# Optimization experiments

Hardware: AMD Instinct MI355X
Metric: run time of the kernel (lower is better)

The kernel has to match this reference:

```python
import jax, jax.numpy as jnp
import numpy as np

DELTA = 0.1      # delta from __init__
LN_EPS = 1e-5    # torch LayerNorm default eps

B, IN, OUT, E = 256, 512, 512, 256


def setup_inputs() -> dict:
    key = jax.random.key(0)
    ks = jax.random.split(key, 6)
    return {
        "x": jax.random.normal(ks[0], (B, IN), dtype=jnp.float32),
        # nn.init.normal_(std=0.1), shape (out_features, in_features)
        "weights": 0.1 * jax.random.normal(ks[1], (OUT, IN), dtype=jnp.float32),
        # frozen predicate embeddings (in_features, embedding_dim)
        "pred_emb": jax.random.normal(ks[2], (IN, E), dtype=jnp.float32),
        # nn.Linear(E, OUT): weight (OUT, E), bias (OUT,)
        "attn_w": jax.random.uniform(ks[3], (OUT, E), dtype=jnp.float32,
                                      minval=-1.0, maxval=1.0) / np.sqrt(E),
        "attn_b": jax.random.uniform(ks[4], (OUT,), dtype=jnp.float32,
                                      minval=-1.0, maxval=1.0) / np.sqrt(E),
        # nn.LayerNorm(OUT)
        "ln_g": jnp.ones((OUT,), dtype=jnp.float32),
        "ln_b": jnp.zeros((OUT,), dtype=jnp.float32),
    }


def _layernorm(s, g, b):
    mu = s.mean(axis=-1, keepdims=True)
    var = ((s - mu) ** 2).mean(axis=-1, keepdims=True)
    return (s - mu) * jax.lax.rsqrt(var + LN_EPS) * g + b


def reference(x, weights, pred_emb, attn_w, attn_b, ln_g, ln_b):
    # semantic attention gate: batch-invariant, compute once -> (IN, OUT)
    scores = pred_emb @ attn_w.T + attn_b                    # (IN, OUT)
    sig = jax.nn.sigmoid(_layernorm(scores, ln_g, ln_b))     # (IN, OUT)

    xe = x[:, :, None]                                       # (B, IN, 1)
    wt = weights.T[None]                                     # (1, IN, OUT)
    # abs_weight * attn_adjusted, fused elementwise -> (B, IN, OUT)
    aw = jnp.abs(xe * wt) * (sig[None] * xe)

    bias = aw.max(axis=1) - aw.sum(axis=1)                   # CONJUNCTION: max - sum
    return x @ weights.T + DELTA * bias                      # (B, OUT)
```

## Files before the change

kernel.cpp:

```cpp
#include <hip/hip_runtime.h>
#include <math.h>

#define B_   256
#define IN_  512
#define OUT_ 512
#define E_   256
#define DELTA_ 0.1f
#define LN_EPS_ 1e-5f

__global__ __launch_bounds__(512)
void k1_scores_ln_sig(const float* __restrict__ pred_emb,
                      const float* __restrict__ attn_w,
                      const float* __restrict__ attn_b,
                      const float* __restrict__ ln_g,
                      const float* __restrict__ ln_b,
                      const float* __restrict__ weights,
                      float* __restrict__ wA,
                      float* __restrict__ vA) {
    __shared__ float pe[4][E_];
    __shared__ float red[8][4][2];
    __shared__ float smu[4], srs[4];

    const int t    = threadIdx.x;
    const int lane = t & 63;
    const int wid  = t >> 6;
    const int i0   = blockIdx.x * 4;
    const int o    = t;

    #pragma unroll
    for (int k = 0; k < 2; ++k) {
        int p = t + 512 * k;
        pe[p >> 8][p & 255] = pred_emb[(size_t)(i0 + (p >> 8)) * E_ + (p & 255)];
    }
    __syncthreads();

    const float4* p0 = reinterpret_cast<const float4*>(pe[0]);
    const float4* p1 = reinterpret_cast<const float4*>(pe[1]);
    const float4* p2 = reinterpret_cast<const float4*>(pe[2]);
    const float4* p3 = reinterpret_cast<const float4*>(pe[3]);
    const float4* wrow = reinterpret_cast<const float4*>(attn_w + (size_t)o * E_);

    float a0 = 0.f, a1 = 0.f, a2 = 0.f, a3 = 0.f;
    #pragma unroll 8
    for (int e4 = 0; e4 < E_ / 4; ++e4) {
        float4 w4 = wrow[e4];
        float4 q0 = p0[e4];
        float4 q1 = p1[e4];
        float4 q2 = p2[e4];
        float4 q3 = p3[e4];
        a0 += q0.x * w4.x + q0.y * w4.y + q0.z * w4.z + q0.w * w4.w;
        a1 += q1.x * w4.x + q1.y * w4.y + q1.z * w4.z + q1.w * w4.w;
        a2 += q2.x * w4.x + q2.y * w4.y + q2.z * w4.z + q2.w * w4.w;
        a3 += q3.x * w4.x + q3.y * w4.y + q3.z * w4.z + q3.w * w4.w;
    }
    const float bo = attn_b[o];
    a0 += bo; a1 += bo; a2 += bo; a3 += bo;

    {
        float s10 = a0, s20 = a0 * a0;
        float s11 = a1, s21 = a1 * a1;
        float s12 = a2, s22 = a2 * a2;
        float s13 = a3, s23 = a3 * a3;
        #pragma unroll
        for (int off = 32; off > 0; off >>= 1) {
            s10 += __shfl_down(s10, off); s20 += __shfl_down(s20, off);
            s11 += __shfl_down(s11, off); s21 += __shfl_down(s21, off);
            s12 += __shfl_down(s12, off); s22 += __shfl_down(s22, off);
            s13 += __shfl_down(s13, off); s23 += __shfl_down(s23, off);
        }
        if (lane == 0) {
            red[wid][0][0] = s10; red[wid][0][1] = s20;
            red[wid][1][0] = s11; red[wid][1][1] = s21;
            red[wid][2][0] = s12; red[wid][2][1] = s22;
            red[wid][3][0] = s13; red[wid][3][1] = s23;
        }
    }
    __syncthreads();
    if (t < 4) {
        float s1 = 0.f, s2 = 0.f;
        #pragma unroll
        for (int w = 0; w < 8; ++w) { s1 += red[w][t][0]; s2 += red[w][t][1]; }
        float mu  = s1 / (float)OUT_;
        float var = s2 / (float)OUT_ - mu * mu;
        smu[t] = mu;
        srs[t] = rsqrtf(var + LN_EPS_);
    }
    __syncthreads();

    const float g  = ln_g[o];
    const float bb = ln_b[o];
    float z0 = (a0 - smu[0]) * srs[0] * g + bb;
    float z1 = (a1 - smu[1]) * srs[1] * g + bb;
    float z2 = (a2 - smu[2]) * srs[2] * g + bb;
    float z3 = (a3 - smu[3]) * srs[3] * g + bb;
    float sg0 = 1.f / (1.f + expf(-z0));
    float sg1 = 1.f / (1.f + expf(-z1));
    float sg2 = 1.f / (1.f + expf(-z2));
    float sg3 = 1.f / (1.f + expf(-z3));

    float4 w4 = *reinterpret_cast<const float4*>(weights + (size_t)o * IN_ + i0);
    wA[(size_t)(i0 + 0) * OUT_ + o] = w4.x;
    wA[(size_t)(i0 + 1) * OUT_ + o] = w4.y;
    wA[(size_t)(i0 + 2) * OUT_ + o] = w4.z;
    wA[(size_t)(i0 + 3) * OUT_ + o] = w4.w;
    vA[(size_t)(i0 + 0) * OUT_ + o] = DELTA_ * fabsf(w4.x) * sg0;
    vA[(size_t)(i0 + 1) * OUT_ + o] = DELTA_ * fabsf(w4.y) * sg1;
    vA[(size_t)(i0 + 2) * OUT_ + o] = DELTA_ * fabsf(w4.z) * sg2;
    vA[(size_t)(i0 + 3) * OUT_ + o] = DELTA_ * fabsf(w4.w) * sg3;
}

#define K2_SK 8
#define K2_CH 64
#define K2_BO (B_ * OUT_)

__global__ __launch_bounds__(256)
void k2_partials(const float* __restrict__ x,
                 const float* __restrict__ wA,
                 const float* __restrict__ vA,
                 float* __restrict__ plin,
                 float* __restrict__ pmax) {
    __shared__ float4 xs [64 * 17];
    __shared__ float4 wss[64 * 17];
    __shared__ float4 vss[64 * 17];

    const int t  = threadIdx.x;
    const int oq = t & 15;
    const int br = t >> 4;
    const int o0 = blockIdx.x * 64;
    const int b0 = blockIdx.y * 64;
    const int i0 = blockIdx.z * K2_CH;

    #pragma unroll
    for (int k = 0; k < 4; ++k) {
        int p   = t + k * 256;
        int row = p >> 4;
        int c4  = p & 15;
        xs [row * 17 + c4] = *reinterpret_cast<const float4*>(
            x  + (size_t)(b0 + row) * IN_  + i0 + c4 * 4);
        wss[row * 17 + c4] = *reinterpret_cast<const float4*>(
            wA + (size_t)(i0 + row) * OUT_ + o0 + c4 * 4);
        vss[row * 17 + c4] = *reinterpret_cast<const float4*>(
            vA + (size_t)(i0 + row) * OUT_ + o0 + c4 * 4);
    }
    __syncthreads();

    float d[4][4], s[4][4], m[4][4];
    #pragma unroll
    for (int b = 0; b < 4; ++b)
        #pragma unroll
        for (int oo = 0; oo < 4; ++oo) {
            d[b][oo] = 0.f; s[b][oo] = 0.f; m[b][oo] = -INFINITY;
        }

    #pragma unroll 2
    for (int i4 = 0; i4 < K2_CH / 4; ++i4) {
        float4 xv0 = xs[(br +  0) * 17 + i4];
        float4 xv1 = xs[(br + 16) * 17 + i4];
        float4 xv2 = xs[(br + 32) * 17 + i4];
        float4 xv3 = xs[(br + 48) * 17 + i4];
        float xr[4][4] = {{xv0.x, xv0.y, xv0.z, xv0.w},
                          {xv1.x, xv1.y, xv1.z, xv1.w},
                          {xv2.x, xv2.y, xv2.z, xv2.w},
                          {xv3.x, xv3.y, xv3.z, xv3.w}};
        float ur[4][4];
        #pragma unroll
        for (int b = 0; b < 4; ++b)
            #pragma unroll
            for (int ii = 0; ii < 4; ++ii)
                ur[b][ii] = xr[b][ii] * fabsf(xr[b][ii]);

        #pragma unroll
        for (int ii = 0; ii < 4; ++ii) {
            float4 w4 = wss[(i4 * 4 + ii) * 17 + oq];
            float4 v4 = vss[(i4 * 4 + ii) * 17 + oq];
            #pragma unroll
            for (int b = 0; b < 4; ++b) {
                float xb = xr[b][ii];
                float ub = ur[b][ii];
                float p_;
                d[b][0] = fmaf(xb, w4.x, d[b][0]); p_ = ub * v4.x; s[b][0] += p_; m[b][0] = fmaxf(m[b][0], p_);
                d[b][1] = fmaf(xb, w4.y, d[b][1]); p_ = ub * v4.y; s[b][1] += p_; m[b][1] = fmaxf(m[b][1], p_);
                d[b][2] = fmaf(xb, w4.z, d[b][2]); p_ = ub * v4.z; s[b][2] += p_; m[b][2] = fmaxf(m[b][2], p_);
                d[b][3] = fmaf(xb, w4.w, d[b][3]); p_ = ub * v4.w; s[b][3] += p_; m[b][3] = fmaxf(m[b][3], p_);
            }
        }
    }

    #pragma unroll
    for (int b = 0; b < 4; ++b) {
        const int row = b0 + br + 16 * b;
        const size_t idx = ((size_t)blockIdx.z * B_ + row) * OUT_ + o0 + oq * 4;
        *reinterpret_cast<float4*>(plin + idx) =
            make_float4(d[b][0] - s[b][0], d[b][1] - s[b][1],
                        d[b][2] - s[b][2], d[b][3] - s[b][3]);
        *reinterpret_cast<float4*>(pmax + idx) =
            make_float4(m[b][0], m[b][1], m[b][2], m[b][3]);
    }
}

__global__ __launch_bounds__(256)
void k3_combine(const float4* __restrict__ plin4,
                const float4* __restrict__ pmax4,
                float4* __restrict__ out4) {
    const int g = blockIdx.x * 256 + threadIdx.x;
    const int Q = K2_BO / 4;
    float4 l  = plin4[g];
    float4 mx = pmax4[g];
    #pragma unroll
    for (int p = 1; p < K2_SK; ++p) {
        float4 lp = plin4[(size_t)p * Q + g];
        float4 mp = pmax4[(size_t)p * Q + g];
        l.x += lp.x; l.y += lp.y; l.z += lp.z; l.w += lp.w;
        mx.x = fmaxf(mx.x, mp.x); mx.y = fmaxf(mx.y, mp.y);
        mx.z = fmaxf(mx.z, mp.z); mx.w = fmaxf(mx.w, mp.w);
    }
    out4[g] = make_float4(l.x + mx.x, l.y + mx.y, l.z + mx.z, l.w + mx.w);
}

extern "C" void kernel_launch(void* const* d_in, const int* in_sizes, int n_in,
                              void* d_out, int out_size, void* d_ws, size_t ws_size,
                              hipStream_t stream) {
    const float* x        = (const float*)d_in[0];
    const float* weights  = (const float*)d_in[1];
    const float* pred_emb = (const float*)d_in[2];
    const float* attn_w   = (const float*)d_in[3];
    const float* attn_b   = (const float*)d_in[4];
    const float* ln_g     = (const float*)d_in[5];
    const float* ln_b     = (const float*)d_in[6];

    float* wA   = (float*)d_ws;
    float* vA   = wA + (size_t)IN_ * OUT_;
    float* plin = vA + (size_t)IN_ * OUT_;
    float* pmax = plin + (size_t)K2_SK * K2_BO;

    k1_scores_ln_sig<<<IN_ / 4, 512, 0, stream>>>(
        pred_emb, attn_w, attn_b, ln_g, ln_b, weights, wA, vA);

    k2_partials<<<dim3(OUT_ / 64, B_ / 64, K2_SK), 256, 0, stream>>>(
        x, wA, vA, plin, pmax);

    k3_combine<<<K2_BO / 4 / 256, 256, 0, stream>>>(
        (const float4*)plin, (const float4*)pmax, (float4*)d_out);
}
```

Measured before the change: 99.68 us.

## Fuse split-K combine into partials kernel via last-block atomic counter

Removes the separate combine kernel. Each output tile now keeps an atomic counter, reset by k1, and the last split-K block to finish reduces the 8 partial sums and maxes for that tile. The partials kernel also moves to 512 threads with 2 outputs per thread instead of 4, giving more threads and fewer registers each. This saves one launch and spreads the combine across blocks, at the cost of a threadfence and an atomic per block and a serialized tail reduction in the last block.

```diff
diff --git a/kernel.cpp b/kernel.cpp
--- a/kernel.cpp
+++ b/kernel.cpp
@@ -7,6 +7,10 @@
 #define E_   256
 #define DELTA_ 0.1f
 #define LN_EPS_ 1e-5f
+
+#define K2_SK 8
+#define K2_CH 64
+#define K2_BO (B_ * OUT_)
 
 __global__ __launch_bounds__(512)
 void k1_scores_ln_sig(const float* __restrict__ pred_emb,
@@ -16,7 +20,8 @@
                       const float* __restrict__ ln_b,
                       const float* __restrict__ weights,
                       float* __restrict__ wA,
-                      float* __restrict__ vA) {
+                      float* __restrict__ vA,
+                      int* __restrict__ cnt) {
     __shared__ float pe[4][E_];
     __shared__ float red[8][4][2];
     __shared__ float smu[4], srs[4];
@@ -26,6 +31,8 @@
     const int wid  = t >> 6;
     const int i0   = blockIdx.x * 4;
     const int o    = t;
+
+    if (blockIdx.x == 0 && t < 32) cnt[t] = 0;
 
     #pragma unroll
     for (int k = 0; k < 2; ++k) {
@@ -109,30 +116,30 @@
     vA[(size_t)(i0 + 3) * OUT_ + o] = DELTA_ * fabsf(w4.w) * sg3;
 }
 
-#define K2_SK 8
-#define K2_CH 64
-#define K2_BO (B_ * OUT_)
-
-__global__ __launch_bounds__(256)
-void k2_partials(const float* __restrict__ x,
-                 const float* __restrict__ wA,
-                 const float* __restrict__ vA,
-                 float* __restrict__ plin,
-                 float* __restrict__ pmax) {
+__global__ __launch_bounds__(512)
+void k2_fused(const float* __restrict__ x,
+              const float* __restrict__ wA,
+              const float* __restrict__ vA,
+              float* __restrict__ plin,
+              float* __restrict__ pmax,
+              int* __restrict__ cnt,
+              float* __restrict__ out) {
     __shared__ float4 xs [64 * 17];
     __shared__ float4 wss[64 * 17];
     __shared__ float4 vss[64 * 17];
+    __shared__ int isLast;
 
     const int t  = threadIdx.x;
-    const int oq = t & 15;
-    const int br = t >> 4;
+    const int oq = t & 31;
+    const int br = t >> 5;
     const int o0 = blockIdx.x * 64;
     const int b0 = blockIdx.y * 64;
-    const int i0 = blockIdx.z * K2_CH;
-
-    #pragma unroll
-    for (int k = 0; k < 4; ++k) {
-        int p   = t + k * 256;
+    const int sk = blockIdx.z;
+    const int i0 = sk * K2_CH;
+
+    #pragma unroll
+    for (int k = 0; k < 2; ++k) {
+        int p   = t + k * 512;
         int row = p >> 4;
         int c4  = p & 15;
         xs [row * 17 + c4] = *reinterpret_cast<const float4*>(
@@ -144,11 +151,14 @@
     }
     __syncthreads();
 
-    float d[4][4], s[4][4], m[4][4];
+    const float2* wf2 = reinterpret_cast<const float2*>(wss);
+    const float2* vf2 = reinterpret_cast<const float2*>(vss);
+
+    float d[4][2], s[4][2], m[4][2];
     #pragma unroll
     for (int b = 0; b < 4; ++b)
         #pragma unroll
-        for (int oo = 0; oo < 4; ++oo) {
+        for (int oo = 0; oo < 2; ++oo) {
             d[b][oo] = 0.f; s[b][oo] = 0.f; m[b][oo] = -INFINITY;
         }
 
@@ -171,50 +181,60 @@
 
         #pragma unroll
         for (int ii = 0; ii < 4; ++ii) {
-            float4 w4 = wss[(i4 * 4 + ii) * 17 + oq];
-            float4 v4 = vss[(i4 * 4 + ii) * 17 + oq];
+            float2 w2 = wf2[(i4 * 4 + ii) * 34 + oq];
+            float2 v2 = vf2[(i4 * 4 + ii) * 34 + oq];
             #pragma unroll
             for (int b = 0; b < 4; ++b) {
                 float xb = xr[b][ii];
                 float ub = ur[b][ii];
                 float p_;
-                d[b][0] = fmaf(xb, w4.x, d[b][0]); p_ = ub * v4.x; s[b][0] += p_; m[b][0] = fmaxf(m[b][0], p_);
-                d[b][1] = fmaf(xb, w4.y, d[b][1]); p_ = ub * v4.y; s[b][1] += p_; m[b][1] = fmaxf(m[b][1], p_);
-                d[b][2] = fmaf(xb, w4.z, d[b][2]); p_ = ub * v4.z; s[b][2] += p_; m[b][2] = fmaxf(m[b][2], p_);
-                d[b][3] = fmaf(xb, w4.w, d[b][3]); p_ = ub * v4.w; s[b][3] += p_; m[b][3] = fmaxf(m[b][3], p_);
+                d[b][0] = fmaf(xb, w2.x, d[b][0]); p_ = ub * v2.x; s[b][0] += p_; m[b][0] = fmaxf(m[b][0], p_);
+                d[b][1] = fmaf(xb, w2.y, d[b][1]); p_ = ub * v2.y; s[b][1] += p_; m[b][1] = fmaxf(m[b][1], p_);
             }
         }
     }
 
     #pragma unroll
     for (int b = 0; b < 4; ++b) {
-        const int row = b0 + br + 16 * b;
-        const size_t idx = ((size_t)blockIdx.z * B_ + row) * OUT_ + o0 + oq * 4;
-        *reinterpret_cast<float4*>(plin + idx) =
-            make_float4(d[b][0] - s[b][0], d[b][1] - s[b][1],
-                        d[b][2] - s[b][2], d[b][3] - s[b][3]);
-        *reinterpret_cast<float4*>(pmax + idx) =
-            make_float4(m[b][0], m[b][1], m[b][2], m[b][3]);
-    }
-}
-
-__global__ __launch_bounds__(256)
-void k3_combine(const float4* __restrict__ plin4,
-                const float4* __restrict__ pmax4,
-                float4* __restrict__ out4) {
-    const int g = blockIdx.x * 256 + threadIdx.x;
+        const int row = br + 16 * b;
+        const size_t idx = ((size_t)sk * B_ + b0 + row) * OUT_ + o0 + oq * 2;
+        *reinterpret_cast<float2*>(plin + idx) =
+            make_float2(d[b][0] - s[b][0], d[b][1] - s[b][1]);
+        *reinterpret_cast<float2*>(pmax + idx) =
+            make_float2(m[b][0], m[b][1]);
+    }
+
+    __threadfence();
+    __syncthreads();
+    if (t == 0)
+        isLast = (atomicAdd(&cnt[blockIdx.y * 8 + blockIdx.x], 1) == K2_SK - 1);
+    __syncthreads();
+    if (!isLast) return;
+    __threadfence();
+
+    const float4* pl4 = reinterpret_cast<const float4*>(plin);
+    const float4* pm4 = reinterpret_cast<const float4*>(pmax);
+    float4* out4 = reinterpret_cast<float4*>(out);
     const int Q = K2_BO / 4;
-    float4 l  = plin4[g];
-    float4 mx = pmax4[g];
-    #pragma unroll
-    for (int p = 1; p < K2_SK; ++p) {
-        float4 lp = plin4[(size_t)p * Q + g];
-        float4 mp = pmax4[(size_t)p * Q + g];
-        l.x += lp.x; l.y += lp.y; l.z += lp.z; l.w += lp.w;
-        mx.x = fmaxf(mx.x, mp.x); mx.y = fmaxf(mx.y, mp.y);
-        mx.z = fmaxf(mx.z, mp.z); mx.w = fmaxf(mx.w, mp.w);
-    }
-    out4[g] = make_float4(l.x + mx.x, l.y + mx.y, l.z + mx.z, l.w + mx.w);
+
+    #pragma unroll
+    for (int k = 0; k < 2; ++k) {
+        int p   = t + k * 512;
+        int row = b0 + (p >> 4);
+        int c4  = (o0 >> 2) + (p & 15);
+        size_t base = (size_t)row * (OUT_ / 4) + c4;
+        float4 l  = pl4[base];
+        float4 mx = pm4[base];
+        #pragma unroll
+        for (int q = 1; q < K2_SK; ++q) {
+            float4 lp = pl4[(size_t)q * Q + base];
+            float4 mp = pm4[(size_t)q * Q + base];
+            l.x += lp.x; l.y += lp.y; l.z += lp.z; l.w += lp.w;
+            mx.x = fmaxf(mx.x, mp.x); mx.y = fmaxf(mx.y, mp.y);
+            mx.z = fmaxf(mx.z, mp.z); mx.w = fmaxf(mx.w, mp.w);
+        }
+        out4[base] = make_float4(l.x + mx.x, l.y + mx.y, l.z + mx.z, l.w + mx.w);
+    }
 }
 
 extern "C" void kernel_launch(void* const* d_in, const int* in_sizes, int n_in,
@@ -232,13 +252,11 @@
     float* vA   = wA + (size_t)IN_ * OUT_;
     float* plin = vA + (size_t)IN_ * OUT_;
     float* pmax = plin + (size_t)K2_SK * K2_BO;
+    int*   cnt  = (int*)(pmax + (size_t)K2_SK * K2_BO);
 
     k1_scores_ln_sig<<<IN_ / 4, 512, 0, stream>>>(
-        pred_emb, attn_w, attn_b, ln_g, ln_b, weights, wA, vA);
-
-    k2_partials<<<dim3(OUT_ / 64, B_ / 64, K2_SK), 256, 0, stream>>>(
-        x, wA, vA, plin, pmax);
-
-    k3_combine<<<K2_BO / 4 / 256, 256, 0, stream>>>(
-        (const float4*)plin, (const float4*)pmax, (float4*)d_out);
+        pred_emb, attn_w, attn_b, ln_g, ln_b, weights, wA, vA, cnt);
+
+    k2_fused<<<dim3(OUT_ / 64, B_ / 64, K2_SK), 512, 0, stream>>>(
+        x, wA, vA, plin, pmax, cnt, (float*)d_out);
 }
```

Result: slower. 153.6 us (+54.1%).
